# Optimization experiments

Hardware: AMD Instinct MI355X
Metric: run time of the kernel (lower is better)

Reference implementation:

```python
import jax, jax.numpy as jnp
import numpy as np

D_MODEL = 1024


def setup_inputs() -> dict:
    key = jax.random.key(0)
    k_x, k_qkv, k_proj, k_b = jax.random.split(key, 4)
    b, t, d = 4, 2048, D_MODEL
    scale = 1.0 / np.sqrt(d)
    x = jax.random.normal(k_x, (b, t, d), dtype=jnp.float32)
    # torch Linear(d, 3d, bias=False): weight [3d, d]; we store transposed [d, 3d]
    w_qkv = jax.random.normal(k_qkv, (d, 3 * d), dtype=jnp.float32) * scale
    w_proj = jax.random.normal(k_proj, (d, d), dtype=jnp.float32) * scale
    b_proj = jax.random.normal(k_b, (d,), dtype=jnp.float32) * scale
    return {"x": x, "w_qkv": w_qkv, "w_proj": w_proj, "b_proj": b_proj}


def reference(x, w_qkv, w_proj, b_proj):
    b, t, d = x.shape
    qkv = jnp.einsum("btd,de->bte", x, w_qkv)  # [b, t, 3d]
    q, k, v = jnp.split(qkv, 3, axis=-1)
    att = jnp.einsum("btd,bsd->bts", q, k) / jnp.sqrt(jnp.float32(d))  # [b, t, t]
    causal = jnp.tril(jnp.ones((t, t), dtype=bool))
    att = jnp.where(causal, att, -jnp.inf)
    att = jax.nn.softmax(att, axis=-1)
    out = jnp.einsum("bts,bsd->btd", att, v)
    return jnp.einsum("btd,de->bte", out, w_proj) + b_proj
```

## Files before the change

kernel.cpp:

```cpp
#include <hip/hip_runtime.h>


typedef __bf16 bf16x8_t __attribute__((ext_vector_type(8)));
typedef float  f32x4_t  __attribute__((ext_vector_type(4)));
typedef unsigned short u16;

struct alignas(8) u16x4 { u16 x, y, z, w; };

__device__ inline float bf2f(u16 u) {
  union { unsigned u; float f; } c; c.u = ((unsigned)u) << 16; return c.f;
}
__device__ inline u16 f2bf(float f) {
  union { float f; unsigned u; } c; c.f = f;
  unsigned r = c.u + 0x7fffu + ((c.u >> 16) & 1u);
  return (u16)(r >> 16);
}

template<int OUTMODE, int GRIDMODE>
__global__ __launch_bounds__(256, 4)
void gemm_bt(const u16* __restrict__ A, const u16* __restrict__ B,
             void* __restrict__ Cv, u16* __restrict__ C2,
             const float* __restrict__ bias,
             int K, int lda, int ldb, int ldc,
             long sA, long sB, long sC)
{
  int bn0, bm0;
  if (GRIDMODE == 1) {
    const int x = blockIdx.x;
    int r = (int)((sqrtf(8.f * x + 1.f) - 1.f) * 0.5f);
    while ((r + 1) * (r + 2) / 2 <= x) ++r;
    while (r * (r + 1) / 2 > x) --r;
    bm0 = r * 128;
    bn0 = (x - r * (r + 1) / 2) * 128;
  } else if (GRIDMODE == 2) {
    bn0 = blockIdx.x * 128;
    const int gy = (int)gridDim.y;
    const int yy = (blockIdx.z & 2) ? (int)blockIdx.y : (gy - 1 - (int)blockIdx.y);
    bm0 = yy * 128;
  } else {
    bn0 = blockIdx.x * 128;
    bm0 = blockIdx.y * 128;
  }
  const long bz = blockIdx.z;
  const u16* Ab = A + bz * sA;
  const u16* Bb = B + bz * sB;
  const int Keff = (GRIDMODE == 2) ? min(K, bm0 + 128) : K;

  __shared__ __align__(16) u16 lA[2 * 128 * 32];
  __shared__ __align__(16) u16 lB[2 * 128 * 32];

  const int tid  = threadIdx.x;
  const int lane = tid & 63;
  const int wv   = tid >> 6;
  const int wm   = (wv >> 1) << 6;
  const int wn   = (wv & 1) << 6;
  const int l15  = lane & 15;
  const int rd_off = l15 * 64 + ((((lane >> 4) ^ (l15 >> 1)) & 3) << 4);

  f32x4_t acc[4][4];
#pragma unroll
  for (int i = 0; i < 4; ++i)
#pragma unroll
    for (int j = 0; j < 4; ++j)
      acc[i][j] = (f32x4_t){0.f, 0.f, 0.f, 0.f};

  float rsacc = 0.f;

  const long ldA2 = (long)lda * 2, ldB2 = (long)ldb * 2;
  const int c_src = (tid & 3) ^ ((tid >> 3) & 3);
  const char* pA = (const char*)(Ab + (long)bm0 * lda) + (long)(tid >> 2) * ldA2 + (c_src << 4);
  const char* pB = (const char*)(Bb + (long)bn0 * ldb) + (long)(tid >> 2) * ldB2 + (c_src << 4);
  const int ldsbo = tid * 16;

  for (int k0 = 0; k0 < Keff; k0 += 64) {
    const long kb = (long)k0 * 2;
#pragma unroll
    for (int r = 0; r < 4; ++r) {
      const long go = (long)(r & 1) * 64 * ldA2 + (r >> 1) * 64;
      __builtin_amdgcn_global_load_lds(
          (const __attribute__((address_space(1))) unsigned int*)(pA + kb + go),
          (__attribute__((address_space(3))) unsigned int*)((char*)lA + ldsbo + r * 4096), 16, 0, 0);
    }
#pragma unroll
    for (int r = 0; r < 4; ++r) {
      const long go = (long)(r & 1) * 64 * ldB2 + (r >> 1) * 64;
      __builtin_amdgcn_global_load_lds(
          (const __attribute__((address_space(1))) unsigned int*)(pB + kb + go),
          (__attribute__((address_space(3))) unsigned int*)((char*)lB + ldsbo + r * 4096), 16, 0, 0);
    }
    __syncthreads();

    const char* lAb = (const char*)lA + wm * 64 + rd_off;
    const char* lBb = (const char*)lB + wn * 64 + rd_off;
#pragma unroll
    for (int s = 0; s < 2; ++s) {
      const int so = s * 8192;
      bf16x8_t b0 = *(const bf16x8_t*)(lBb + so + 0 * 1024);
      bf16x8_t b1 = *(const bf16x8_t*)(lBb + so + 1 * 1024);
      bf16x8_t b2 = *(const bf16x8_t*)(lBb + so + 2 * 1024);
      bf16x8_t b3 = *(const bf16x8_t*)(lBb + so + 3 * 1024);
#pragma unroll
      for (int mf = 0; mf < 4; ++mf) {
        bf16x8_t a = *(const bf16x8_t*)(lAb + so + mf * 1024);
        acc[mf][0] = __builtin_amdgcn_mfma_f32_16x16x32_bf16(a, b0, acc[mf][0], 0, 0, 0);
        acc[mf][1] = __builtin_amdgcn_mfma_f32_16x16x32_bf16(a, b1, acc[mf][1], 0, 0, 0);
        acc[mf][2] = __builtin_amdgcn_mfma_f32_16x16x32_bf16(a, b2, acc[mf][2], 0, 0, 0);
        acc[mf][3] = __builtin_amdgcn_mfma_f32_16x16x32_bf16(a, b3, acc[mf][3], 0, 0, 0);
      }
    }

    if (OUTMODE == 4) {
      const int rr = tid >> 1;
      const int bsel = (tid & 1) * 8192;
#pragma unroll
      for (int c = 0; c < 4; ++c) {
        const int cc = (c + (rr >> 1)) & 3;
        bf16x8_t v = *(const bf16x8_t*)((const char*)lA + bsel + rr * 64 + cc * 16);
#pragma unroll
        for (int e = 0; e < 8; ++e) rsacc += (float)v[e];
      }
    }
    __syncthreads();
  }

  const int r4 = (lane >> 4) << 2;

  if (OUTMODE == 2) {
    if (bn0 >= 2048) {
#pragma unroll
      for (int mf = 0; mf < 4; ++mf) {
        const int s0 = bm0 + wm + mf * 16 + r4;
        const int b_ = s0 >> 11;
        const int s_ = s0 & 2047;
#pragma unroll
        for (int nf = 0; nf < 4; ++nf) {
          const int dcol = bn0 - 2048 + wn + nf * 16 + l15;
          u16x4 o = {f2bf(acc[mf][nf][0]), f2bf(acc[mf][nf][1]),
                     f2bf(acc[mf][nf][2]), f2bf(acc[mf][nf][3])};
          *(u16x4*)&C2[(((long)b_ * 1024 + dcol) << 11) + s_] = o;
        }
      }
    } else {
      u16* Cb16 = (u16*)Cv;
#pragma unroll
      for (int mf = 0; mf < 4; ++mf)
#pragma unroll
        for (int nf = 0; nf < 4; ++nf) {
          const int col = bn0 + wn + nf * 16 + l15;
#pragma unroll
          for (int r = 0; r < 4; ++r)
            Cb16[(long)(bm0 + wm + mf * 16 + r4 + r) * ldc + col] = f2bf(acc[mf][nf][r]);
        }
    }
    return;
  }

  if (OUTMODE == 3) {
    const float scale = 0.03125f;
    const bool diag = (bm0 == bn0);
    u16* Cb16 = (u16*)Cv + bz * sC;
#pragma unroll
    for (int mf = 0; mf < 4; ++mf)
#pragma unroll
      for (int r = 0; r < 4; ++r) {
        const int grow = bm0 + wm + mf * 16 + r4 + r;
#pragma unroll
        for (int nf = 0; nf < 4; ++nf) {
          const int col = bn0 + wn + nf * 16 + l15;
          float e = (diag && col > grow) ? 0.f : __expf(acc[mf][nf][r] * scale);
          Cb16[(long)grow * ldc + col] = f2bf(e);
        }
      }
    return;
  }

  if (OUTMODE == 4) {
    float* rsl = (float*)lA;
    rsl[tid] = rsacc;
    __syncthreads();
    float* rinv = (float*)lB;
    if (tid < 128) rinv[tid] = 1.0f / (rsl[2 * tid] + rsl[2 * tid + 1]);
    __syncthreads();
    u16* Cb16 = (u16*)Cv + bz * sC;
#pragma unroll
    for (int mf = 0; mf < 4; ++mf)
#pragma unroll
      for (int nf = 0; nf < 4; ++nf) {
        const int col = bn0 + wn + nf * 16 + l15;
#pragma unroll
        for (int r = 0; r < 4; ++r) {
          const int rl = wm + mf * 16 + r4 + r;
          Cb16[(long)(bm0 + rl) * ldc + col] = f2bf(acc[mf][nf][r] * rinv[rl]);
        }
      }
    return;
  }

  float* Cf32 = (float*)Cv + bz * sC;
#pragma unroll
  for (int mf = 0; mf < 4; ++mf)
#pragma unroll
    for (int nf = 0; nf < 4; ++nf) {
      const int col = bn0 + wn + nf * 16 + l15;
      const float bb = bias[col];
#pragma unroll
      for (int r = 0; r < 4; ++r)
        Cf32[(long)(bm0 + wm + mf * 16 + r4 + r) * ldc + col] = acc[mf][nf][r] + bb;
    }
}

__global__ __launch_bounds__(256)
void prep(const float* __restrict__ x, u16* __restrict__ xbf,
          const float* __restrict__ wqkv, u16* __restrict__ wqkvT,
          const float* __restrict__ wproj, u16* __restrict__ wprojT) {
  const int bid = blockIdx.x;
  if (bid < 8192) {
    const int i = bid * 256 + threadIdx.x;
    float4 v = ((const float4*)x)[i];
    u16x4 o = {f2bf(v.x), f2bf(v.y), f2bf(v.z), f2bf(v.w)};
    ((u16x4*)xbf)[i] = o;
    return;
  }
  const int tb = bid - 8192;
  const int bx = tb & 127;
  const int by = tb >> 7;
  const bool isq = bx < 96;
  const float* in = isq ? wqkv : wproj;
  u16* out        = isq ? wqkvT : wprojT;
  const int C     = isq ? 3072 : 1024;
  const int c0 = (isq ? bx : (bx - 96)) * 32;
  const int r0 = by * 32;
  __shared__ float t[32][33];
  const int tx = threadIdx.x & 31, ty = threadIdx.x >> 5;
#pragma unroll
  for (int i = 0; i < 32; i += 8)
    t[ty + i][tx] = in[(long)(r0 + ty + i) * C + (c0 + tx)];
  __syncthreads();
#pragma unroll
  for (int i = 0; i < 32; i += 8)
    out[(long)(c0 + ty + i) * 1024 + (r0 + tx)] = f2bf(t[tx][ty + i]);
}

extern "C" void kernel_launch(void* const* d_in, const int* in_sizes, int n_in,
                              void* d_out, int out_size, void* d_ws, size_t ws_size,
                              hipStream_t stream) {
  (void)in_sizes; (void)n_in; (void)out_size; (void)ws_size;
  const float* x      = (const float*)d_in[0];
  const float* w_qkv  = (const float*)d_in[1];
  const float* w_proj = (const float*)d_in[2];
  const float* b_proj = (const float*)d_in[3];
  float* y = (float*)d_out;
  char*  ws = (char*)d_ws;

  u16* xbf    = (u16*)(ws);
  u16* qk     = (u16*)(ws + (16l << 20));
  u16* wqkvT  = (u16*)(ws + (48l << 20));
  u16* wprojT = (u16*)(ws + (54l << 20));
  u16* vT     = (u16*)(ws + (56l << 20));
  u16* E      = (u16*)(ws + (72l << 20));
  u16* attn   = xbf;

  prep<<<12288, 256, 0, stream>>>(x, xbf, w_qkv, wqkvT, w_proj, wprojT);
  gemm_bt<2, 0><<<dim3(24, 64, 1), 256, 0, stream>>>(
      xbf, wqkvT, qk, vT, nullptr, 1024, 1024, 1024, 2048, 0, 0, 0);
  gemm_bt<3, 1><<<dim3(136, 1, 4), 256, 0, stream>>>(
      qk, qk + 1024, E, nullptr, nullptr, 1024, 2048, 2048, 2048,
      (long)2048 * 2048, (long)2048 * 2048, (long)2048 * 2048);
  gemm_bt<4, 2><<<dim3(8, 16, 4), 256, 0, stream>>>(
      E, vT, attn, nullptr, nullptr, 2048, 2048, 2048, 1024,
      (long)2048 * 2048, (long)1024 * 2048, (long)2048 * 1024);
  gemm_bt<1, 0><<<dim3(8, 64, 1), 256, 0, stream>>>(
      attn, wprojT, y, nullptr, b_proj, 1024, 1024, 1024, 1024, 0, 0, 0);
}
```

Before: 259.7 us.

## Fold weight products algebraically to drop the output projection GEMM

```diff
diff --git a/kernel.cpp b/kernel.cpp
--- a/kernel.cpp
+++ b/kernel.cpp
@@ -7,9 +7,6 @@
 
 struct alignas(8) u16x4 { u16 x, y, z, w; };
 
-__device__ inline float bf2f(u16 u) {
-  union { unsigned u; float f; } c; c.u = ((unsigned)u) << 16; return c.f;
-}
 __device__ inline u16 f2bf(float f) {
   union { float f; unsigned u; } c; c.f = f;
   unsigned r = c.u + 0x7fffu + ((c.u >> 16) & 1u);
@@ -19,6 +16,7 @@
 template<int OUTMODE, int GRIDMODE>
 __global__ __launch_bounds__(256, 4)
 void gemm_bt(const u16* __restrict__ A, const u16* __restrict__ B,
+             const u16* __restrict__ B2,
              void* __restrict__ Cv, u16* __restrict__ C2,
              const float* __restrict__ bias,
              int K, int lda, int ldb, int ldc,
@@ -43,7 +41,8 @@
   }
   const long bz = blockIdx.z;
   const u16* Ab = A + bz * sA;
-  const u16* Bb = B + bz * sB;
+  const u16* Bb = ((OUTMODE == 2 && bn0 >= 1024) ? B2 : B) + bz * sB;
+  const int effbn = (OUTMODE == 2) ? (bn0 & 1023) : bn0;
   const int Keff = (GRIDMODE == 2) ? min(K, bm0 + 128) : K;
 
   __shared__ __align__(16) u16 lA[2 * 128 * 32];
@@ -69,7 +68,7 @@
   const long ldA2 = (long)lda * 2, ldB2 = (long)ldb * 2;
   const int c_src = (tid & 3) ^ ((tid >> 3) & 3);
   const char* pA = (const char*)(Ab + (long)bm0 * lda) + (long)(tid >> 2) * ldA2 + (c_src << 4);
-  const char* pB = (const char*)(Bb + (long)bn0 * ldb) + (long)(tid >> 2) * ldB2 + (c_src << 4);
+  const char* pB = (const char*)(Bb + (long)effbn * ldb) + (long)(tid >> 2) * ldB2 + (c_src << 4);
   const int ldsbo = tid * 16;
 
   for (int k0 = 0; k0 < Keff; k0 += 64) {
@@ -126,7 +125,7 @@
   const int r4 = (lane >> 4) << 2;
 
   if (OUTMODE == 2) {
-    if (bn0 >= 2048) {
+    if (bn0 >= 1024) {
 #pragma unroll
       for (int mf = 0; mf < 4; ++mf) {
         const int s0 = bm0 + wm + mf * 16 + r4;
@@ -134,10 +133,10 @@
         const int s_ = s0 & 2047;
 #pragma unroll
         for (int nf = 0; nf < 4; ++nf) {
-          const int dcol = bn0 - 2048 + wn + nf * 16 + l15;
+          const int ocol = bn0 - 1024 + wn + nf * 16 + l15;
           u16x4 o = {f2bf(acc[mf][nf][0]), f2bf(acc[mf][nf][1]),
                      f2bf(acc[mf][nf][2]), f2bf(acc[mf][nf][3])};
-          *(u16x4*)&C2[(((long)b_ * 1024 + dcol) << 11) + s_] = o;
+          *(u16x4*)&C2[(((long)b_ * 1024 + ocol) << 11) + s_] = o;
         }
       }
     } else {
@@ -181,37 +180,114 @@
     float* rinv = (float*)lB;
     if (tid < 128) rinv[tid] = 1.0f / (rsl[2 * tid] + rsl[2 * tid + 1]);
     __syncthreads();
-    u16* Cb16 = (u16*)Cv + bz * sC;
+    float* Yf = (float*)Cv + bz * sC;
 #pragma unroll
     for (int mf = 0; mf < 4; ++mf)
 #pragma unroll
       for (int nf = 0; nf < 4; ++nf) {
         const int col = bn0 + wn + nf * 16 + l15;
+        const float bb = bias[col];
 #pragma unroll
         for (int r = 0; r < 4; ++r) {
           const int rl = wm + mf * 16 + r4 + r;
-          Cb16[(long)(bm0 + rl) * ldc + col] = f2bf(acc[mf][nf][r] * rinv[rl]);
+          Yf[(long)(bm0 + rl) * ldc + col] = acc[mf][nf][r] * rinv[rl] + bb;
         }
       }
     return;
   }
-
-  float* Cf32 = (float*)Cv + bz * sC;
+}
+
+__global__ __launch_bounds__(256, 4)
+void gemm_w(const u16* __restrict__ wfull, const u16* __restrict__ wprojT,
+            u16* __restrict__ WqkT, u16* __restrict__ W2vT)
+{
+  const bool g2 = blockIdx.y >= 8;
+  const int bm0 = ((int)blockIdx.y & 7) * 128;
+  const int bn0 = (int)blockIdx.x * 128;
+  const u16* A = g2 ? wprojT : (wfull + 1024);
+  const u16* B = g2 ? (wfull + 2048) : wfull;
+  const int lda = g2 ? 1024 : 3072;
+  const int ldb = 3072;
+  u16* C = g2 ? W2vT : WqkT;
+
+  __shared__ __align__(16) u16 lA[2 * 128 * 32];
+  __shared__ __align__(16) u16 lB[2 * 128 * 32];
+
+  const int tid  = threadIdx.x;
+  const int lane = tid & 63;
+  const int wv   = tid >> 6;
+  const int wm   = (wv >> 1) << 6;
+  const int wn   = (wv & 1) << 6;
+  const int l15  = lane & 15;
+  const int rd_off = l15 * 64 + ((((lane >> 4) ^ (l15 >> 1)) & 3) << 4);
+
+  f32x4_t acc[4][4];
+#pragma unroll
+  for (int i = 0; i < 4; ++i)
+#pragma unroll
+    for (int j = 0; j < 4; ++j)
+      acc[i][j] = (f32x4_t){0.f, 0.f, 0.f, 0.f};
+
+  const long ldA2 = (long)lda * 2, ldB2 = (long)ldb * 2;
+  const int c_src = (tid & 3) ^ ((tid >> 3) & 3);
+  const char* pA = (const char*)(A + (long)bm0 * lda) + (long)(tid >> 2) * ldA2 + (c_src << 4);
+  const char* pB = (const char*)(B + (long)bn0 * ldb) + (long)(tid >> 2) * ldB2 + (c_src << 4);
+  const int ldsbo = tid * 16;
+
+  for (int k0 = 0; k0 < 1024; k0 += 64) {
+    const long kb = (long)k0 * 2;
+#pragma unroll
+    for (int r = 0; r < 4; ++r) {
+      const long go = (long)(r & 1) * 64 * ldA2 + (r >> 1) * 64;
+      __builtin_amdgcn_global_load_lds(
+          (const __attribute__((address_space(1))) unsigned int*)(pA + kb + go),
+          (__attribute__((address_space(3))) unsigned int*)((char*)lA + ldsbo + r * 4096), 16, 0, 0);
+    }
+#pragma unroll
+    for (int r = 0; r < 4; ++r) {
+      const long go = (long)(r & 1) * 64 * ldB2 + (r >> 1) * 64;
+      __builtin_amdgcn_global_load_lds(
+          (const __attribute__((address_space(1))) unsigned int*)(pB + kb + go),
+          (__attribute__((address_space(3))) unsigned int*)((char*)lB + ldsbo + r * 4096), 16, 0, 0);
+    }
+    __syncthreads();
+
+    const char* lAb = (const char*)lA + wm * 64 + rd_off;
+    const char* lBb = (const char*)lB + wn * 64 + rd_off;
+#pragma unroll
+    for (int s = 0; s < 2; ++s) {
+      const int so = s * 8192;
+      bf16x8_t b0 = *(const bf16x8_t*)(lBb + so + 0 * 1024);
+      bf16x8_t b1 = *(const bf16x8_t*)(lBb + so + 1 * 1024);
+      bf16x8_t b2 = *(const bf16x8_t*)(lBb + so + 2 * 1024);
+      bf16x8_t b3 = *(const bf16x8_t*)(lBb + so + 3 * 1024);
+#pragma unroll
+      for (int mf = 0; mf < 4; ++mf) {
+        bf16x8_t a = *(const bf16x8_t*)(lAb + so + mf * 1024);
+        acc[mf][0] = __builtin_amdgcn_mfma_f32_16x16x32_bf16(a, b0, acc[mf][0], 0, 0, 0);
+        acc[mf][1] = __builtin_amdgcn_mfma_f32_16x16x32_bf16(a, b1, acc[mf][1], 0, 0, 0);
+        acc[mf][2] = __builtin_amdgcn_mfma_f32_16x16x32_bf16(a, b2, acc[mf][2], 0, 0, 0);
+        acc[mf][3] = __builtin_amdgcn_mfma_f32_16x16x32_bf16(a, b3, acc[mf][3], 0, 0, 0);
+      }
+    }
+    __syncthreads();
+  }
+
+  const int r4 = (lane >> 4) << 2;
 #pragma unroll
   for (int mf = 0; mf < 4; ++mf)
 #pragma unroll
     for (int nf = 0; nf < 4; ++nf) {
       const int col = bn0 + wn + nf * 16 + l15;
-      const float bb = bias[col];
 #pragma unroll
       for (int r = 0; r < 4; ++r)
-        Cf32[(long)(bm0 + wm + mf * 16 + r4 + r) * ldc + col] = acc[mf][nf][r] + bb;
+        C[(long)(bm0 + wm + mf * 16 + r4 + r) * 1024 + col] = f2bf(acc[mf][nf][r]);
     }
 }
 
 __global__ __launch_bounds__(256)
 void prep(const float* __restrict__ x, u16* __restrict__ xbf,
-          const float* __restrict__ wqkv, u16* __restrict__ wqkvT,
+          const float* __restrict__ wqkv, u16* __restrict__ wfull,
           const float* __restrict__ wproj, u16* __restrict__ wprojT) {
   const int bid = blockIdx.x;
   if (bid < 8192) {
@@ -221,24 +297,25 @@
     ((u16x4*)xbf)[i] = o;
     return;
   }
-  const int tb = bid - 8192;
-  const int bx = tb & 127;
-  const int by = tb >> 7;
-  const bool isq = bx < 96;
-  const float* in = isq ? wqkv : wproj;
-  u16* out        = isq ? wqkvT : wprojT;
-  const int C     = isq ? 3072 : 1024;
-  const int c0 = (isq ? bx : (bx - 96)) * 32;
-  const int r0 = by * 32;
-  __shared__ float t[32][33];
-  const int tx = threadIdx.x & 31, ty = threadIdx.x >> 5;
-#pragma unroll
-  for (int i = 0; i < 32; i += 8)
-    t[ty + i][tx] = in[(long)(r0 + ty + i) * C + (c0 + tx)];
-  __syncthreads();
-#pragma unroll
-  for (int i = 0; i < 32; i += 8)
-    out[(long)(c0 + ty + i) * 1024 + (r0 + tx)] = f2bf(t[tx][ty + i]);
+  if (bid < 9216) {
+    const int tb = bid - 8192;
+    const int c0 = (tb & 31) * 32;
+    const int r0 = (tb >> 5) * 32;
+    __shared__ float t[32][33];
+    const int tx = threadIdx.x & 31, ty = threadIdx.x >> 5;
+#pragma unroll
+    for (int i = 0; i < 32; i += 8)
+      t[ty + i][tx] = wproj[(long)(r0 + ty + i) * 1024 + (c0 + tx)];
+    __syncthreads();
+#pragma unroll
+    for (int i = 0; i < 32; i += 8)
+      wprojT[(long)(c0 + ty + i) * 1024 + (r0 + tx)] = f2bf(t[tx][ty + i]);
+    return;
+  }
+  const int i = (bid - 9216) * 256 + threadIdx.x;
+  float4 v = ((const float4*)wqkv)[i];
+  u16x4 o = {f2bf(v.x), f2bf(v.y), f2bf(v.z), f2bf(v.w)};
+  ((u16x4*)wfull)[i] = o;
 }
 
 extern "C" void kernel_launch(void* const* d_in, const int* in_sizes, int n_in,
@@ -253,22 +330,22 @@
   char*  ws = (char*)d_ws;
 
   u16* xbf    = (u16*)(ws);
-  u16* qk     = (u16*)(ws + (16l << 20));
-  u16* wqkvT  = (u16*)(ws + (48l << 20));
-  u16* wprojT = (u16*)(ws + (54l << 20));
-  u16* vT     = (u16*)(ws + (56l << 20));
-  u16* E      = (u16*)(ws + (72l << 20));
-  u16* attn   = xbf;
-
-  prep<<<12288, 256, 0, stream>>>(x, xbf, w_qkv, wqkvT, w_proj, wprojT);
-  gemm_bt<2, 0><<<dim3(24, 64, 1), 256, 0, stream>>>(
-      xbf, wqkvT, qk, vT, nullptr, 1024, 1024, 1024, 2048, 0, 0, 0);
+  u16* t1     = (u16*)(ws + (16l << 20));
+  u16* WqkT   = (u16*)(ws + (32l << 20));
+  u16* W2vT   = (u16*)(ws + (34l << 20));
+  u16* wprojT = (u16*)(ws + (36l << 20));
+  u16* wfull  = (u16*)(ws + (38l << 20));
+  u16* VWT    = (u16*)(ws + (44l << 20));
+  u16* E      = (u16*)(ws + (60l << 20));
+
+  prep<<<12288, 256, 0, stream>>>(x, xbf, w_qkv, wfull, w_proj, wprojT);
+  gemm_w<<<dim3(8, 16), 256, 0, stream>>>(wfull, wprojT, WqkT, W2vT);
+  gemm_bt<2, 0><<<dim3(16, 64, 1), 256, 0, stream>>>(
+      xbf, WqkT, W2vT, t1, VWT, nullptr, 1024, 1024, 1024, 1024, 0, 0, 0);
   gemm_bt<3, 1><<<dim3(136, 1, 4), 256, 0, stream>>>(
-      qk, qk + 1024, E, nullptr, nullptr, 1024, 2048, 2048, 2048,
-      (long)2048 * 2048, (long)2048 * 2048, (long)2048 * 2048);
+      t1, xbf, nullptr, E, nullptr, nullptr, 1024, 1024, 1024, 2048,
+      (long)2048 * 1024, (long)2048 * 1024, (long)2048 * 2048);
   gemm_bt<4, 2><<<dim3(8, 16, 4), 256, 0, stream>>>(
-      E, vT, attn, nullptr, nullptr, 2048, 2048, 2048, 1024,
+      E, VWT, nullptr, y, nullptr, b_proj, 2048, 2048, 2048, 1024,
       (long)2048 * 2048, (long)1024 * 2048, (long)2048 * 1024);
-  gemm_bt<1, 0><<<dim3(8, 64, 1), 256, 0, stream>>>(
-      attn, wprojT, y, nullptr, b_proj, 1024, 1024, 1024, 1024, 0, 0, 0);
-}
+}
```

Result: faster. 238.3 us (-8.2%).
